# Optimization experiments

Measured on AMD Instinct MI355X. Metric: run time of the kernel, lower is better.

## Reference

```python
import jax, jax.numpy as jnp
import numpy as np

N_NODES = 20000
LN_EPS = 1e-5


def setup_inputs() -> dict:
    key = jax.random.key(0)
    ks = jax.random.split(key, 8)
    N, E, D_IN, D_H = N_NODES, 320000, 128, 256
    x = jax.random.normal(ks[0], (N, D_IN), dtype=jnp.float32)
    edge_index = jax.random.randint(ks[1], (2, E), 0, N, dtype=jnp.int64)
    edge_weight = jax.random.uniform(ks[2], (E,), dtype=jnp.float32)
    # Glorot-ish scaled weights
    W1 = jax.random.normal(ks[3], (D_IN, D_H), dtype=jnp.float32) / np.sqrt(D_IN)
    W2 = jax.random.normal(ks[4], (D_H, D_H), dtype=jnp.float32) / np.sqrt(D_H)
    Wres = jax.random.normal(ks[5], (D_IN, D_H), dtype=jnp.float32) / np.sqrt(D_IN)
    return {
        "x": x, "edge_index": edge_index, "edge_weight": edge_weight,
        "W1": W1, "b1": jnp.zeros((D_H,), jnp.float32),
        "W2": W2, "b2": jnp.zeros((D_H,), jnp.float32),
        "Wres": Wres, "bres": jnp.zeros((D_H,), jnp.float32),
        "gamma1": jnp.ones((D_H,), jnp.float32), "beta1": jnp.zeros((D_H,), jnp.float32),
        "gamma2": jnp.ones((D_H,), jnp.float32), "beta2": jnp.zeros((D_H,), jnp.float32),
    }


def _gcn_conv(x, W, b, src, dst, w, n):
    # PyG GCNConv: linear transform, then sym-normalized scatter-add aggregation
    h = x @ W  # [N, D_H]
    deg = jax.ops.segment_sum(w, dst, num_segments=n)  # in-degree incl. self loops
    dinv = jnp.where(deg > 0, jax.lax.rsqrt(deg), 0.0)
    norm = dinv[src] * w * dinv[dst]  # [E+N]
    out = jax.ops.segment_sum(norm[:, None] * h[src], dst, num_segments=n)
    return out + b


def _layer_norm(x, gamma, beta):
    mu = jnp.mean(x, axis=-1, keepdims=True)
    var = jnp.mean(jnp.square(x - mu), axis=-1, keepdims=True)
    return (x - mu) * jax.lax.rsqrt(var + LN_EPS) * gamma + beta


def reference(x, edge_index, edge_weight, W1, b1, W2, b2, Wres, bres,
              gamma1, beta1, gamma2, beta2):
    n = x.shape[0]
    loop = jnp.arange(n, dtype=edge_index.dtype)
    # add self loops with weight 1 (add_self_loops=True)
    src = jnp.concatenate([edge_index[0], loop])
    dst = jnp.concatenate([edge_index[1], loop])
    w = jnp.concatenate([edge_weight, jnp.ones((n,), edge_weight.dtype)])

    # hop 0: conv -> relu (dropout p=0, eval) -> residual proj -> LayerNorm
    delta = jax.nn.relu(_gcn_conv(x, W1, b1, src, dst, w, n))
    h = _layer_norm(x @ Wres + bres + delta, gamma1, beta1)

    # hop 1 (last): conv -> residual -> LayerNorm (no relu)
    delta = _gcn_conv(h, W2, b2, src, dst, w, n)
    h = _layer_norm(h + delta, gamma2, beta2)
    return h
```

## Files before the change

kernel.cpp:

```cpp
#include <hip/hip_runtime.h>
#include <stdint.h>


constexpr int DIN = 128;
constexpr int DH  = 256;
#define LN_EPS 1e-5f

typedef __attribute__((ext_vector_type(8))) short bf16x8;
typedef __attribute__((ext_vector_type(4))) short bf16x4;
typedef __attribute__((ext_vector_type(4))) float f32x4;

__device__ __forceinline__ short f2bf(float f) {
  union { float f; unsigned u; } v; v.f = f;
  unsigned r = v.u + 0x7fffu + ((v.u >> 16) & 1u);
  return (short)(r >> 16);
}
__device__ __forceinline__ float bf2f(short b) {
  union { unsigned u; float f; } v; v.u = ((unsigned)(unsigned short)b) << 16;
  return v.f;
}

__device__ __forceinline__ int probe_m64(const unsigned* ei, int E) {
  int lane = threadIdx.x & 63;
  long long stride = (E >= 64) ? (E / 64) : 1;
  long long li = (long long)lane * stride;
  if (li >= E) li = 0;
  unsigned v = ei[2 * li + 1];
  return __ballot(v != 0u) == 0ull;
}

__device__ __forceinline__ int eidx(const void* ei, long long e, int m64) {
  return m64 ? (int)((const long long*)ei)[e] : ((const int*)ei)[e];
}


__global__ __launch_bounds__(256) void k_prep(const float* __restrict__ x,
                                              short* __restrict__ xb,
                                              const float* __restrict__ W1,
                                              const float* __restrict__ Wres,
                                              const float* __restrict__ W2,
                                              short* __restrict__ W1t,
                                              short* __restrict__ Wrt,
                                              short* __restrict__ W2t,
                                              const void* ei,
                                              const float* __restrict__ ew,
                                              float* deg, int* cnt,
                                              int N, int E) {
  const int NXV = N * DIN / 8;
  const int NW  = DIN * DH;
  const int NW2 = DH * DH;
  int idx = blockIdx.x * 256 + threadIdx.x;
  if (idx < NXV) {
    f32x4 a = ((const f32x4*)x)[idx * 2];
    f32x4 b = ((const f32x4*)x)[idx * 2 + 1];
    bf16x8 o;
    o[0] = f2bf(a[0]); o[1] = f2bf(a[1]); o[2] = f2bf(a[2]); o[3] = f2bf(a[3]);
    o[4] = f2bf(b[0]); o[5] = f2bf(b[1]); o[6] = f2bf(b[2]); o[7] = f2bf(b[3]);
    ((bf16x8*)xb)[idx] = o;
    return;
  }
  idx -= NXV;
  if (idx < NW) {
    int n = idx / DIN, k = idx % DIN;
    W1t[idx] = f2bf(W1[k * DH + n]);
    return;
  }
  idx -= NW;
  if (idx < NW) {
    int n = idx / DIN, k = idx % DIN;
    Wrt[idx] = f2bf(Wres[k * DH + n]);
    return;
  }
  idx -= NW;
  if (idx < NW2) {
    int n = idx / DH, k = idx % DH;
    W2t[idx] = f2bf(W2[k * DH + n]);
    return;
  }
  idx -= NW2;
  int m64 = probe_m64((const unsigned*)ei, E);
  if (idx < E) {
    int d = eidx(ei, (long long)E + idx, m64);
    atomicAdd(&deg[d], ew[idx]);
    atomicAdd(&cnt[d], 1);
  }
}


__global__ __launch_bounds__(1024) void k_scan(const int* __restrict__ cnt,
                                               float* deg, int* rowptr,
                                               int* cursor, int n) {
  for (int i = threadIdx.x; i < n; i += 1024) deg[i] = rsqrtf(1.0f + deg[i]);

  constexpr int MAXI = 32;
  int items = (n + 1023) / 1024;
  int tid = threadIdx.x, lane = tid & 63, wv = tid >> 6;
  int base = tid * items;
  int v[MAXI];
  int tot = 0;
#pragma unroll 4
  for (int j = 0; j < items; ++j) {
    int i = base + j;
    v[j] = (i < n) ? cnt[i] : 0;
    tot += v[j];
  }
  int sc = tot;
#pragma unroll
  for (int off = 1; off < 64; off <<= 1) {
    int t = __shfl_up(sc, off, 64);
    if (lane >= off) sc += t;
  }
  __shared__ int wsum[16];
  if (lane == 63) wsum[wv] = sc;
  __syncthreads();
  if (wv == 0 && lane < 16) {
    int s = wsum[lane];
#pragma unroll
    for (int off = 1; off < 16; off <<= 1) {
      int t = __shfl_up(s, off, 64);
      if (lane >= off) s += t;
    }
    wsum[lane] = s;
  }
  __syncthreads();
  int prefix = (sc - tot) + ((wv > 0) ? wsum[wv - 1] : 0);
  if (tid == 0) { rowptr[0] = 0; cursor[0] = 0; }
  int run = prefix;
#pragma unroll 4
  for (int j = 0; j < items; ++j) {
    int i = base + j;
    run += v[j];
    if (i < n) { rowptr[i + 1] = run; cursor[i + 1] = run; }
  }
}


__global__ __launch_bounds__(256) void k_gemm_l1_fill(
    const short* __restrict__ A, const short* __restrict__ B1,
    const short* __restrict__ Br, const float* __restrict__ bres,
    short* __restrict__ H1, short* __restrict__ RESb, int M, int MB,
    const void* ei, const float* __restrict__ ew,
    const float* __restrict__ dinv, int* cursor, int* srcs, float* norms,
    int E) {
  constexpr int K = DIN;
  int GB = MB * 4;
  if ((int)blockIdx.x >= GB) {
    int m64 = probe_m64((const unsigned*)ei, E);
    int e = ((int)blockIdx.x - GB) * 256 + threadIdx.x;
    if (e >= E) return;
    int s = eidx(ei, e, m64);
    int d = eidx(ei, (long long)E + e, m64);
    int p = atomicAdd(&cursor[d], 1);
    srcs[p] = s;
    norms[p] = dinv[s] * ew[e] * dinv[d];
    return;
  }
  int mb = (int)blockIdx.x % MB, nbk = (int)blockIdx.x / MB;
  int tid = threadIdx.x;
  int wave = tid >> 6, lane = tid & 63;
  int lr = lane & 15, lg = lane >> 4;
  int bm = mb * 64 + (wave >> 1) * 32;
  int bn = nbk * 64 + (wave & 1) * 32;

  int r0 = min(bm + lr, M - 1);
  int r1 = min(bm + 16 + lr, M - 1);
  const short* a0p = A + (long long)r0 * K + lg * 8;
  const short* a1p = A + (long long)r1 * K + lg * 8;
  const short* b10p = B1 + (long long)(bn + lr) * K + lg * 8;
  const short* b11p = B1 + (long long)(bn + 16 + lr) * K + lg * 8;
  const short* br0p = Br + (long long)(bn + lr) * K + lg * 8;
  const short* br1p = Br + (long long)(bn + 16 + lr) * K + lg * 8;

  f32x4 a1c[2][2] = {}, arc[2][2] = {};
#pragma unroll
  for (int ks = 0; ks < K / 32; ++ks) {
    bf16x8 a0 = *(const bf16x8*)(a0p + ks * 32);
    bf16x8 a1 = *(const bf16x8*)(a1p + ks * 32);
    bf16x8 p0 = *(const bf16x8*)(b10p + ks * 32);
    bf16x8 p1 = *(const bf16x8*)(b11p + ks * 32);
    bf16x8 q0 = *(const bf16x8*)(br0p + ks * 32);
    bf16x8 q1 = *(const bf16x8*)(br1p + ks * 32);
    a1c[0][0] = __builtin_amdgcn_mfma_f32_16x16x32_bf16(a0, p0, a1c[0][0], 0, 0, 0);
    a1c[0][1] = __builtin_amdgcn_mfma_f32_16x16x32_bf16(a0, p1, a1c[0][1], 0, 0, 0);
    a1c[1][0] = __builtin_amdgcn_mfma_f32_16x16x32_bf16(a1, p0, a1c[1][0], 0, 0, 0);
    a1c[1][1] = __builtin_amdgcn_mfma_f32_16x16x32_bf16(a1, p1, a1c[1][1], 0, 0, 0);
    arc[0][0] = __builtin_amdgcn_mfma_f32_16x16x32_bf16(a0, q0, arc[0][0], 0, 0, 0);
    arc[0][1] = __builtin_amdgcn_mfma_f32_16x16x32_bf16(a0, q1, arc[0][1], 0, 0, 0);
    arc[1][0] = __builtin_amdgcn_mfma_f32_16x16x32_bf16(a1, q0, arc[1][0], 0, 0, 0);
    arc[1][1] = __builtin_amdgcn_mfma_f32_16x16x32_bf16(a1, q1, arc[1][1], 0, 0, 0);
  }

#pragma unroll
  for (int mi = 0; mi < 2; ++mi)
#pragma unroll
    for (int ni = 0; ni < 2; ++ni)
#pragma unroll
      for (int j = 0; j < 4; ++j) {
        int row = bm + mi * 16 + lg * 4 + j;
        int col = bn + ni * 16 + lr;
        if (row < M) {
          H1[(long long)row * DH + col] = f2bf(a1c[mi][ni][j]);
          RESb[(long long)row * DH + col] = f2bf(arc[mi][ni][j] + bres[col]);
        }
      }
}


__global__ __launch_bounds__(256) void k_gemm2(const short* __restrict__ A,
                                               const short* __restrict__ Bt,
                                               short* __restrict__ outb, int M) {
  constexpr int K = DH;
  int tid = threadIdx.x;
  int wave = tid >> 6, lane = tid & 63;
  int lr = lane & 15, lg = lane >> 4;
  int bm = blockIdx.x * 64 + (wave >> 1) * 32;
  int bn = blockIdx.y * 64 + (wave & 1) * 32;

  int r0 = min(bm + lr, M - 1);
  int r1 = min(bm + 16 + lr, M - 1);
  const short* a0p = A + (long long)r0 * K + lg * 8;
  const short* a1p = A + (long long)r1 * K + lg * 8;
  const short* b0p = Bt + (long long)(bn + lr) * K + lg * 8;
  const short* b1p = Bt + (long long)(bn + 16 + lr) * K + lg * 8;

  f32x4 acc[2][2] = {};
#pragma unroll
  for (int ks = 0; ks < K / 32; ++ks) {
    bf16x8 a0 = *(const bf16x8*)(a0p + ks * 32);
    bf16x8 a1 = *(const bf16x8*)(a1p + ks * 32);
    bf16x8 b0 = *(const bf16x8*)(b0p + ks * 32);
    bf16x8 b1 = *(const bf16x8*)(b1p + ks * 32);
    acc[0][0] = __builtin_amdgcn_mfma_f32_16x16x32_bf16(a0, b0, acc[0][0], 0, 0, 0);
    acc[0][1] = __builtin_amdgcn_mfma_f32_16x16x32_bf16(a0, b1, acc[0][1], 0, 0, 0);
    acc[1][0] = __builtin_amdgcn_mfma_f32_16x16x32_bf16(a1, b0, acc[1][0], 0, 0, 0);
    acc[1][1] = __builtin_amdgcn_mfma_f32_16x16x32_bf16(a1, b1, acc[1][1], 0, 0, 0);
  }

#pragma unroll
  for (int mi = 0; mi < 2; ++mi)
#pragma unroll
    for (int ni = 0; ni < 2; ++ni)
#pragma unroll
      for (int j = 0; j < 4; ++j) {
        int row = bm + mi * 16 + lg * 4 + j;
        int col = bn + ni * 16 + lr;
        if (row < M) outb[(long long)row * DH + col] = f2bf(acc[mi][ni][j]);
      }
}


template <bool RELU, bool RESBF>
__global__ __launch_bounds__(256) void k_agg_ln(
    const short* __restrict__ H, const void* __restrict__ resid,
    const float* __restrict__ bias, const float* __restrict__ gamma,
    const float* __restrict__ beta, const int* __restrict__ rowptr,
    const int* __restrict__ srcs, const float* __restrict__ norms,
    const float* __restrict__ dinv, float* __restrict__ out_f,
    short* __restrict__ out_bf, int n) {
  int wv = threadIdx.x >> 6, lane = threadIdx.x & 63;
  int i = blockIdx.x * 4 + wv;
  if (i >= n) return;
  int d = lane * 4;

  float di = dinv[i];
  float acc0, acc1, acc2, acc3;
  {
    bf16x4 hv = *(const bf16x4*)(H + (long long)i * DH + d);
    float sw = di * di;
    acc0 = sw * bf2f(hv[0]); acc1 = sw * bf2f(hv[1]);
    acc2 = sw * bf2f(hv[2]); acc3 = sw * bf2f(hv[3]);
  }
  int e = rowptr[i], end = rowptr[i + 1];
  for (; e + 8 <= end; e += 8) {
    int s0 = srcs[e],     s1 = srcs[e + 1], s2 = srcs[e + 2], s3 = srcs[e + 3];
    int s4 = srcs[e + 4], s5 = srcs[e + 5], s6 = srcs[e + 6], s7 = srcs[e + 7];
    bf16x4 v0 = *(const bf16x4*)(H + (long long)s0 * DH + d);
    bf16x4 v1 = *(const bf16x4*)(H + (long long)s1 * DH + d);
    bf16x4 v2 = *(const bf16x4*)(H + (long long)s2 * DH + d);
    bf16x4 v3 = *(const bf16x4*)(H + (long long)s3 * DH + d);
    bf16x4 v4 = *(const bf16x4*)(H + (long long)s4 * DH + d);
    bf16x4 v5 = *(const bf16x4*)(H + (long long)s5 * DH + d);
    bf16x4 v6 = *(const bf16x4*)(H + (long long)s6 * DH + d);
    bf16x4 v7 = *(const bf16x4*)(H + (long long)s7 * DH + d);
    float n0 = norms[e],     n1 = norms[e + 1], n2 = norms[e + 2], n3 = norms[e + 3];
    float n4 = norms[e + 4], n5 = norms[e + 5], n6 = norms[e + 6], n7 = norms[e + 7];
    acc0 += n0 * bf2f(v0[0]); acc1 += n0 * bf2f(v0[1]);
    acc2 += n0 * bf2f(v0[2]); acc3 += n0 * bf2f(v0[3]);
    acc0 += n1 * bf2f(v1[0]); acc1 += n1 * bf2f(v1[1]);
    acc2 += n1 * bf2f(v1[2]); acc3 += n1 * bf2f(v1[3]);
    acc0 += n2 * bf2f(v2[0]); acc1 += n2 * bf2f(v2[1]);
    acc2 += n2 * bf2f(v2[2]); acc3 += n2 * bf2f(v2[3]);
    acc0 += n3 * bf2f(v3[0]); acc1 += n3 * bf2f(v3[1]);
    acc2 += n3 * bf2f(v3[2]); acc3 += n3 * bf2f(v3[3]);
    acc0 += n4 * bf2f(v4[0]); acc1 += n4 * bf2f(v4[1]);
    acc2 += n4 * bf2f(v4[2]); acc3 += n4 * bf2f(v4[3]);
    acc0 += n5 * bf2f(v5[0]); acc1 += n5 * bf2f(v5[1]);
    acc2 += n5 * bf2f(v5[2]); acc3 += n5 * bf2f(v5[3]);
    acc0 += n6 * bf2f(v6[0]); acc1 += n6 * bf2f(v6[1]);
    acc2 += n6 * bf2f(v6[2]); acc3 += n6 * bf2f(v6[3]);
    acc0 += n7 * bf2f(v7[0]); acc1 += n7 * bf2f(v7[1]);
    acc2 += n7 * bf2f(v7[2]); acc3 += n7 * bf2f(v7[3]);
  }
  for (; e < end; ++e) {
    int s = srcs[e];
    float nm = norms[e];
    bf16x4 v = *(const bf16x4*)(H + (long long)s * DH + d);
    acc0 += nm * bf2f(v[0]); acc1 += nm * bf2f(v[1]);
    acc2 += nm * bf2f(v[2]); acc3 += nm * bf2f(v[3]);
  }

  float r0, r1, r2, r3;
  if (RESBF) {
    bf16x4 rv = *(const bf16x4*)((const short*)resid + (long long)i * DH + d);
    r0 = bf2f(rv[0]); r1 = bf2f(rv[1]); r2 = bf2f(rv[2]); r3 = bf2f(rv[3]);
  } else {
    f32x4 rv = *(const f32x4*)((const float*)resid + (long long)i * DH + d);
    r0 = rv[0]; r1 = rv[1]; r2 = rv[2]; r3 = rv[3];
  }
  f32x4 bv = *(const f32x4*)(bias + d);
  float t0 = acc0 + bv[0], t1 = acc1 + bv[1], t2 = acc2 + bv[2], t3 = acc3 + bv[3];
  if (RELU) {
    t0 = fmaxf(t0, 0.f); t1 = fmaxf(t1, 0.f);
    t2 = fmaxf(t2, 0.f); t3 = fmaxf(t3, 0.f);
  }
  t0 += r0; t1 += r1; t2 += r2; t3 += r3;

  float s1 = t0 + t1 + t2 + t3;
  float s2 = t0 * t0 + t1 * t1 + t2 * t2 + t3 * t3;
#pragma unroll
  for (int m = 1; m < 64; m <<= 1) {
    s1 += __shfl_xor(s1, m, 64);
    s2 += __shfl_xor(s2, m, 64);
  }
  float mu = s1 * (1.f / 256.f);
  float var = s2 * (1.f / 256.f) - mu * mu;
  float rs = rsqrtf(var + LN_EPS);

  f32x4 gv = *(const f32x4*)(gamma + d);
  f32x4 be = *(const f32x4*)(beta + d);
  f32x4 y;
  y[0] = (t0 - mu) * rs * gv[0] + be[0];
  y[1] = (t1 - mu) * rs * gv[1] + be[1];
  y[2] = (t2 - mu) * rs * gv[2] + be[2];
  y[3] = (t3 - mu) * rs * gv[3] + be[3];
  if (out_f) *(f32x4*)(out_f + (long long)i * DH + d) = y;
  if (out_bf) {
    bf16x4 ob;
    ob[0] = f2bf(y[0]); ob[1] = f2bf(y[1]);
    ob[2] = f2bf(y[2]); ob[3] = f2bf(y[3]);
    *(bf16x4*)(out_bf + (long long)i * DH + d) = ob;
  }
}


extern "C" void kernel_launch(void* const* d_in, const int* in_sizes, int n_in,
                              void* d_out, int out_size, void* d_ws,
                              size_t ws_size, hipStream_t stream) {
  const float* x    = (const float*)d_in[0];
  const void*  ei   = d_in[1];
  const float* ew   = (const float*)d_in[2];
  const float* W1   = (const float*)d_in[3];
  const float* b1   = (const float*)d_in[4];
  const float* W2   = (const float*)d_in[5];
  const float* b2   = (const float*)d_in[6];
  const float* Wres = (const float*)d_in[7];
  const float* bres = (const float*)d_in[8];
  const float* g1   = (const float*)d_in[9];
  const float* be1  = (const float*)d_in[10];
  const float* g2   = (const float*)d_in[11];
  const float* be2  = (const float*)d_in[12];

  const int N = in_sizes[0] / DIN;
  const int E = in_sizes[2];

  char* ws = (char*)d_ws;
  auto alloc = [&](size_t bytes) -> char* {
    char* p = ws;
    ws += (bytes + 255) & ~(size_t)255;
    return p;
  };
  short* xb     = (short*)alloc((size_t)N * DIN * 2);
  short* W1t    = (short*)alloc((size_t)DIN * DH * 2);
  short* Wrt    = (short*)alloc((size_t)DIN * DH * 2);
  short* W2t    = (short*)alloc((size_t)DH * DH * 2);
  short* Hb     = (short*)alloc((size_t)N * DH * 2);
  short* RESb   = (short*)alloc((size_t)N * DH * 2);
  short* h1b    = (short*)alloc((size_t)N * DH * 2);
  int*   cnt    = (int*)alloc((size_t)N * 8);
  float* deg    = (float*)(cnt + N);
  int*   rowptr = (int*)alloc((size_t)(N + 1) * 4);
  int*   cursor = (int*)alloc((size_t)(N + 1) * 4);
  int*   srcs   = (int*)alloc((size_t)E * 4);
  float* norms  = (float*)alloc((size_t)E * 4);

  hipMemsetAsync(cnt, 0, (size_t)N * 8, stream);

  int prep_items = N * DIN / 8 + 2 * DIN * DH + DH * DH + E;
  k_prep<<<(prep_items + 255) / 256, 256, 0, stream>>>(
      x, xb, W1, Wres, W2, W1t, Wrt, W2t, ei, ew, deg, cnt, N, E);
  k_scan<<<1, 1024, 0, stream>>>(cnt, deg, rowptr, cursor, N);

  const int MB = (N + 63) / 64;
  const int FB = (E + 255) / 256;
  k_gemm_l1_fill<<<MB * 4 + FB, 256, 0, stream>>>(
      xb, W1t, Wrt, bres, Hb, RESb, N, MB, ei, ew, deg, cursor, srcs, norms, E);
  k_agg_ln<true, true><<<(N + 3) / 4, 256, 0, stream>>>(
      Hb, RESb, b1, g1, be1, rowptr, srcs, norms, deg, nullptr, h1b, N);

  dim3 gg(MB, DH / 64);
  k_gemm2<<<gg, 256, 0, stream>>>(h1b, W2t, Hb, N);
  k_agg_ln<false, true><<<(N + 3) / 4, 256, 0, stream>>>(
      Hb, h1b, b2, g2, be2, rowptr, srcs, norms, deg, (float*)d_out, nullptr, N);
}
```

Before: 265.1 us.

## Aggregate before transform and fuse GEMM with bias, residual and LayerNorm

Reorders each GCN layer so aggregation runs first, using linearity (A·X·W = (A·X)·W). For layer 1 this gathers the 128-wide input instead of the 256-wide hidden, halving gather traffic. The dense GEMMs now use one wave per 16 rows covering all 256 columns, so bias, ReLU, the residual projection and LayerNorm all finish in registers, with no HBM round-trip for intermediates or separate aggregation+LN kernels. The CSR fill moves to its own kernel, and the aggregation kernels split each row's edges across two half-waves. The trade-offs are low-occupancy 64-thread GEMM blocks that reload weights from global memory per block, and bf16 rounding of the aggregated features.

```diff
diff --git a/kernel.cpp b/kernel.cpp
--- a/kernel.cpp
+++ b/kernel.cpp
@@ -135,220 +135,233 @@
 }
 
 
-__global__ __launch_bounds__(256) void k_gemm_l1_fill(
-    const short* __restrict__ A, const short* __restrict__ B1,
-    const short* __restrict__ Br, const float* __restrict__ bres,
-    short* __restrict__ H1, short* __restrict__ RESb, int M, int MB,
-    const void* ei, const float* __restrict__ ew,
-    const float* __restrict__ dinv, int* cursor, int* srcs, float* norms,
-    int E) {
-  constexpr int K = DIN;
-  int GB = MB * 4;
-  if ((int)blockIdx.x >= GB) {
-    int m64 = probe_m64((const unsigned*)ei, E);
-    int e = ((int)blockIdx.x - GB) * 256 + threadIdx.x;
-    if (e >= E) return;
-    int s = eidx(ei, e, m64);
-    int d = eidx(ei, (long long)E + e, m64);
-    int p = atomicAdd(&cursor[d], 1);
-    srcs[p] = s;
-    norms[p] = dinv[s] * ew[e] * dinv[d];
-    return;
-  }
-  int mb = (int)blockIdx.x % MB, nbk = (int)blockIdx.x / MB;
-  int tid = threadIdx.x;
-  int wave = tid >> 6, lane = tid & 63;
-  int lr = lane & 15, lg = lane >> 4;
-  int bm = mb * 64 + (wave >> 1) * 32;
-  int bn = nbk * 64 + (wave & 1) * 32;
-
-  int r0 = min(bm + lr, M - 1);
-  int r1 = min(bm + 16 + lr, M - 1);
-  const short* a0p = A + (long long)r0 * K + lg * 8;
-  const short* a1p = A + (long long)r1 * K + lg * 8;
-  const short* b10p = B1 + (long long)(bn + lr) * K + lg * 8;
-  const short* b11p = B1 + (long long)(bn + 16 + lr) * K + lg * 8;
-  const short* br0p = Br + (long long)(bn + lr) * K + lg * 8;
-  const short* br1p = Br + (long long)(bn + 16 + lr) * K + lg * 8;
-
-  f32x4 a1c[2][2] = {}, arc[2][2] = {};
-#pragma unroll
-  for (int ks = 0; ks < K / 32; ++ks) {
-    bf16x8 a0 = *(const bf16x8*)(a0p + ks * 32);
-    bf16x8 a1 = *(const bf16x8*)(a1p + ks * 32);
-    bf16x8 p0 = *(const bf16x8*)(b10p + ks * 32);
-    bf16x8 p1 = *(const bf16x8*)(b11p + ks * 32);
-    bf16x8 q0 = *(const bf16x8*)(br0p + ks * 32);
-    bf16x8 q1 = *(const bf16x8*)(br1p + ks * 32);
-    a1c[0][0] = __builtin_amdgcn_mfma_f32_16x16x32_bf16(a0, p0, a1c[0][0], 0, 0, 0);
-    a1c[0][1] = __builtin_amdgcn_mfma_f32_16x16x32_bf16(a0, p1, a1c[0][1], 0, 0, 0);
-    a1c[1][0] = __builtin_amdgcn_mfma_f32_16x16x32_bf16(a1, p0, a1c[1][0], 0, 0, 0);
-    a1c[1][1] = __builtin_amdgcn_mfma_f32_16x16x32_bf16(a1, p1, a1c[1][1], 0, 0, 0);
-    arc[0][0] = __builtin_amdgcn_mfma_f32_16x16x32_bf16(a0, q0, arc[0][0], 0, 0, 0);
-    arc[0][1] = __builtin_amdgcn_mfma_f32_16x16x32_bf16(a0, q1, arc[0][1], 0, 0, 0);
-    arc[1][0] = __builtin_amdgcn_mfma_f32_16x16x32_bf16(a1, q0, arc[1][0], 0, 0, 0);
-    arc[1][1] = __builtin_amdgcn_mfma_f32_16x16x32_bf16(a1, q1, arc[1][1], 0, 0, 0);
-  }
-
-#pragma unroll
-  for (int mi = 0; mi < 2; ++mi)
-#pragma unroll
-    for (int ni = 0; ni < 2; ++ni)
-#pragma unroll
-      for (int j = 0; j < 4; ++j) {
-        int row = bm + mi * 16 + lg * 4 + j;
-        int col = bn + ni * 16 + lr;
-        if (row < M) {
-          H1[(long long)row * DH + col] = f2bf(a1c[mi][ni][j]);
-          RESb[(long long)row * DH + col] = f2bf(arc[mi][ni][j] + bres[col]);
-        }
-      }
-}
-
-
-__global__ __launch_bounds__(256) void k_gemm2(const short* __restrict__ A,
-                                               const short* __restrict__ Bt,
-                                               short* __restrict__ outb, int M) {
-  constexpr int K = DH;
-  int tid = threadIdx.x;
-  int wave = tid >> 6, lane = tid & 63;
-  int lr = lane & 15, lg = lane >> 4;
-  int bm = blockIdx.x * 64 + (wave >> 1) * 32;
-  int bn = blockIdx.y * 64 + (wave & 1) * 32;
-
-  int r0 = min(bm + lr, M - 1);
-  int r1 = min(bm + 16 + lr, M - 1);
-  const short* a0p = A + (long long)r0 * K + lg * 8;
-  const short* a1p = A + (long long)r1 * K + lg * 8;
-  const short* b0p = Bt + (long long)(bn + lr) * K + lg * 8;
-  const short* b1p = Bt + (long long)(bn + 16 + lr) * K + lg * 8;
-
-  f32x4 acc[2][2] = {};
-#pragma unroll
-  for (int ks = 0; ks < K / 32; ++ks) {
-    bf16x8 a0 = *(const bf16x8*)(a0p + ks * 32);
-    bf16x8 a1 = *(const bf16x8*)(a1p + ks * 32);
-    bf16x8 b0 = *(const bf16x8*)(b0p + ks * 32);
-    bf16x8 b1 = *(const bf16x8*)(b1p + ks * 32);
-    acc[0][0] = __builtin_amdgcn_mfma_f32_16x16x32_bf16(a0, b0, acc[0][0], 0, 0, 0);
-    acc[0][1] = __builtin_amdgcn_mfma_f32_16x16x32_bf16(a0, b1, acc[0][1], 0, 0, 0);
-    acc[1][0] = __builtin_amdgcn_mfma_f32_16x16x32_bf16(a1, b0, acc[1][0], 0, 0, 0);
-    acc[1][1] = __builtin_amdgcn_mfma_f32_16x16x32_bf16(a1, b1, acc[1][1], 0, 0, 0);
-  }
-
-#pragma unroll
-  for (int mi = 0; mi < 2; ++mi)
-#pragma unroll
-    for (int ni = 0; ni < 2; ++ni)
-#pragma unroll
-      for (int j = 0; j < 4; ++j) {
-        int row = bm + mi * 16 + lg * 4 + j;
-        int col = bn + ni * 16 + lr;
-        if (row < M) outb[(long long)row * DH + col] = f2bf(acc[mi][ni][j]);
-      }
-}
-
-
-template <bool RELU, bool RESBF>
-__global__ __launch_bounds__(256) void k_agg_ln(
-    const short* __restrict__ H, const void* __restrict__ resid,
-    const float* __restrict__ bias, const float* __restrict__ gamma,
-    const float* __restrict__ beta, const int* __restrict__ rowptr,
-    const int* __restrict__ srcs, const float* __restrict__ norms,
-    const float* __restrict__ dinv, float* __restrict__ out_f,
-    short* __restrict__ out_bf, int n) {
+__global__ __launch_bounds__(256) void k_fill(const void* ei,
+                                              const float* __restrict__ w,
+                                              const float* __restrict__ dinv,
+                                              int* cursor, int* srcs,
+                                              float* norms, int E) {
+  int m64 = probe_m64((const unsigned*)ei, E);
+  int e = blockIdx.x * 256 + threadIdx.x;
+  if (e >= E) return;
+  int s = eidx(ei, e, m64);
+  int d = eidx(ei, (long long)E + e, m64);
+  int p = atomicAdd(&cursor[d], 1);
+  srcs[p] = s;
+  norms[p] = dinv[s] * w[e] * dinv[d];
+}
+
+
+__global__ __launch_bounds__(256) void k_agg128(const short* __restrict__ T,
+                                                const int* __restrict__ rowptr,
+                                                const int* __restrict__ srcs,
+                                                const float* __restrict__ norms,
+                                                const float* __restrict__ dinv,
+                                                short* __restrict__ out, int n) {
   int wv = threadIdx.x >> 6, lane = threadIdx.x & 63;
   int i = blockIdx.x * 4 + wv;
   if (i >= n) return;
-  int d = lane * 4;
-
-  float di = dinv[i];
-  float acc0, acc1, acc2, acc3;
-  {
-    bf16x4 hv = *(const bf16x4*)(H + (long long)i * DH + d);
-    float sw = di * di;
-    acc0 = sw * bf2f(hv[0]); acc1 = sw * bf2f(hv[1]);
-    acc2 = sw * bf2f(hv[2]); acc3 = sw * bf2f(hv[3]);
-  }
-  int e = rowptr[i], end = rowptr[i + 1];
-  for (; e + 8 <= end; e += 8) {
-    int s0 = srcs[e],     s1 = srcs[e + 1], s2 = srcs[e + 2], s3 = srcs[e + 3];
-    int s4 = srcs[e + 4], s5 = srcs[e + 5], s6 = srcs[e + 6], s7 = srcs[e + 7];
-    bf16x4 v0 = *(const bf16x4*)(H + (long long)s0 * DH + d);
-    bf16x4 v1 = *(const bf16x4*)(H + (long long)s1 * DH + d);
-    bf16x4 v2 = *(const bf16x4*)(H + (long long)s2 * DH + d);
-    bf16x4 v3 = *(const bf16x4*)(H + (long long)s3 * DH + d);
-    bf16x4 v4 = *(const bf16x4*)(H + (long long)s4 * DH + d);
-    bf16x4 v5 = *(const bf16x4*)(H + (long long)s5 * DH + d);
-    bf16x4 v6 = *(const bf16x4*)(H + (long long)s6 * DH + d);
-    bf16x4 v7 = *(const bf16x4*)(H + (long long)s7 * DH + d);
-    float n0 = norms[e],     n1 = norms[e + 1], n2 = norms[e + 2], n3 = norms[e + 3];
-    float n4 = norms[e + 4], n5 = norms[e + 5], n6 = norms[e + 6], n7 = norms[e + 7];
-    acc0 += n0 * bf2f(v0[0]); acc1 += n0 * bf2f(v0[1]);
-    acc2 += n0 * bf2f(v0[2]); acc3 += n0 * bf2f(v0[3]);
-    acc0 += n1 * bf2f(v1[0]); acc1 += n1 * bf2f(v1[1]);
-    acc2 += n1 * bf2f(v1[2]); acc3 += n1 * bf2f(v1[3]);
-    acc0 += n2 * bf2f(v2[0]); acc1 += n2 * bf2f(v2[1]);
-    acc2 += n2 * bf2f(v2[2]); acc3 += n2 * bf2f(v2[3]);
-    acc0 += n3 * bf2f(v3[0]); acc1 += n3 * bf2f(v3[1]);
-    acc2 += n3 * bf2f(v3[2]); acc3 += n3 * bf2f(v3[3]);
-    acc0 += n4 * bf2f(v4[0]); acc1 += n4 * bf2f(v4[1]);
-    acc2 += n4 * bf2f(v4[2]); acc3 += n4 * bf2f(v4[3]);
-    acc0 += n5 * bf2f(v5[0]); acc1 += n5 * bf2f(v5[1]);
-    acc2 += n5 * bf2f(v5[2]); acc3 += n5 * bf2f(v5[3]);
-    acc0 += n6 * bf2f(v6[0]); acc1 += n6 * bf2f(v6[1]);
-    acc2 += n6 * bf2f(v6[2]); acc3 += n6 * bf2f(v6[3]);
-    acc0 += n7 * bf2f(v7[0]); acc1 += n7 * bf2f(v7[1]);
-    acc2 += n7 * bf2f(v7[2]); acc3 += n7 * bf2f(v7[3]);
-  }
-  for (; e < end; ++e) {
+  int h = lane >> 5;
+  int c = (lane & 31) * 4;
+  float a0 = 0.f, a1 = 0.f, a2 = 0.f, a3 = 0.f;
+  int e = rowptr[i] + h, end = rowptr[i + 1];
+  for (; e + 6 < end; e += 8) {
+    int s0 = srcs[e], s1 = srcs[e + 2], s2 = srcs[e + 4], s3 = srcs[e + 6];
+    float w0 = norms[e], w1 = norms[e + 2], w2 = norms[e + 4], w3 = norms[e + 6];
+    bf16x4 v0 = *(const bf16x4*)(T + (long long)s0 * DIN + c);
+    bf16x4 v1 = *(const bf16x4*)(T + (long long)s1 * DIN + c);
+    bf16x4 v2 = *(const bf16x4*)(T + (long long)s2 * DIN + c);
+    bf16x4 v3 = *(const bf16x4*)(T + (long long)s3 * DIN + c);
+    a0 += w0 * bf2f(v0[0]) + w1 * bf2f(v1[0]) + w2 * bf2f(v2[0]) + w3 * bf2f(v3[0]);
+    a1 += w0 * bf2f(v0[1]) + w1 * bf2f(v1[1]) + w2 * bf2f(v2[1]) + w3 * bf2f(v3[1]);
+    a2 += w0 * bf2f(v0[2]) + w1 * bf2f(v1[2]) + w2 * bf2f(v2[2]) + w3 * bf2f(v3[2]);
+    a3 += w0 * bf2f(v0[3]) + w1 * bf2f(v1[3]) + w2 * bf2f(v2[3]) + w3 * bf2f(v3[3]);
+  }
+  for (; e < end; e += 2) {
     int s = srcs[e];
-    float nm = norms[e];
-    bf16x4 v = *(const bf16x4*)(H + (long long)s * DH + d);
-    acc0 += nm * bf2f(v[0]); acc1 += nm * bf2f(v[1]);
-    acc2 += nm * bf2f(v[2]); acc3 += nm * bf2f(v[3]);
-  }
-
-  float r0, r1, r2, r3;
-  if (RESBF) {
-    bf16x4 rv = *(const bf16x4*)((const short*)resid + (long long)i * DH + d);
-    r0 = bf2f(rv[0]); r1 = bf2f(rv[1]); r2 = bf2f(rv[2]); r3 = bf2f(rv[3]);
-  } else {
-    f32x4 rv = *(const f32x4*)((const float*)resid + (long long)i * DH + d);
-    r0 = rv[0]; r1 = rv[1]; r2 = rv[2]; r3 = rv[3];
-  }
-  f32x4 bv = *(const f32x4*)(bias + d);
-  float t0 = acc0 + bv[0], t1 = acc1 + bv[1], t2 = acc2 + bv[2], t3 = acc3 + bv[3];
-  if (RELU) {
-    t0 = fmaxf(t0, 0.f); t1 = fmaxf(t1, 0.f);
-    t2 = fmaxf(t2, 0.f); t3 = fmaxf(t3, 0.f);
-  }
-  t0 += r0; t1 += r1; t2 += r2; t3 += r3;
-
-  float s1 = t0 + t1 + t2 + t3;
-  float s2 = t0 * t0 + t1 * t1 + t2 * t2 + t3 * t3;
-#pragma unroll
-  for (int m = 1; m < 64; m <<= 1) {
-    s1 += __shfl_xor(s1, m, 64);
-    s2 += __shfl_xor(s2, m, 64);
-  }
-  float mu = s1 * (1.f / 256.f);
-  float var = s2 * (1.f / 256.f) - mu * mu;
-  float rs = rsqrtf(var + LN_EPS);
-
-  f32x4 gv = *(const f32x4*)(gamma + d);
-  f32x4 be = *(const f32x4*)(beta + d);
-  f32x4 y;
-  y[0] = (t0 - mu) * rs * gv[0] + be[0];
-  y[1] = (t1 - mu) * rs * gv[1] + be[1];
-  y[2] = (t2 - mu) * rs * gv[2] + be[2];
-  y[3] = (t3 - mu) * rs * gv[3] + be[3];
-  if (out_f) *(f32x4*)(out_f + (long long)i * DH + d) = y;
-  if (out_bf) {
-    bf16x4 ob;
-    ob[0] = f2bf(y[0]); ob[1] = f2bf(y[1]);
-    ob[2] = f2bf(y[2]); ob[3] = f2bf(y[3]);
-    *(bf16x4*)(out_bf + (long long)i * DH + d) = ob;
+    float w = norms[e];
+    bf16x4 v = *(const bf16x4*)(T + (long long)s * DIN + c);
+    a0 += w * bf2f(v[0]); a1 += w * bf2f(v[1]);
+    a2 += w * bf2f(v[2]); a3 += w * bf2f(v[3]);
+  }
+  a0 += __shfl_xor(a0, 32, 64); a1 += __shfl_xor(a1, 32, 64);
+  a2 += __shfl_xor(a2, 32, 64); a3 += __shfl_xor(a3, 32, 64);
+  if (h == 0) {
+    float sw = dinv[i] * dinv[i];
+    bf16x4 sv = *(const bf16x4*)(T + (long long)i * DIN + c);
+    bf16x4 o;
+    o[0] = f2bf(a0 + sw * bf2f(sv[0]));
+    o[1] = f2bf(a1 + sw * bf2f(sv[1]));
+    o[2] = f2bf(a2 + sw * bf2f(sv[2]));
+    o[3] = f2bf(a3 + sw * bf2f(sv[3]));
+    *(bf16x4*)(out + (long long)i * DIN + c) = o;
+  }
+}
+
+__global__ __launch_bounds__(256) void k_agg256(const short* __restrict__ T,
+                                                const int* __restrict__ rowptr,
+                                                const int* __restrict__ srcs,
+                                                const float* __restrict__ norms,
+                                                const float* __restrict__ dinv,
+                                                short* __restrict__ out, int n) {
+  int wv = threadIdx.x >> 6, lane = threadIdx.x & 63;
+  int i = blockIdx.x * 4 + wv;
+  if (i >= n) return;
+  int h = lane >> 5;
+  int c = (lane & 31) * 8;
+  float acc[8];
+#pragma unroll
+  for (int k = 0; k < 8; ++k) acc[k] = 0.f;
+  int e = rowptr[i] + h, end = rowptr[i + 1];
+  for (; e + 6 < end; e += 8) {
+    int s0 = srcs[e], s1 = srcs[e + 2], s2 = srcs[e + 4], s3 = srcs[e + 6];
+    float w0 = norms[e], w1 = norms[e + 2], w2 = norms[e + 4], w3 = norms[e + 6];
+    bf16x8 v0 = *(const bf16x8*)(T + (long long)s0 * DH + c);
+    bf16x8 v1 = *(const bf16x8*)(T + (long long)s1 * DH + c);
+    bf16x8 v2 = *(const bf16x8*)(T + (long long)s2 * DH + c);
+    bf16x8 v3 = *(const bf16x8*)(T + (long long)s3 * DH + c);
+#pragma unroll
+    for (int k = 0; k < 8; ++k)
+      acc[k] += w0 * bf2f(v0[k]) + w1 * bf2f(v1[k]) +
+                w2 * bf2f(v2[k]) + w3 * bf2f(v3[k]);
+  }
+  for (; e < end; e += 2) {
+    int s = srcs[e];
+    float w = norms[e];
+    bf16x8 v = *(const bf16x8*)(T + (long long)s * DH + c);
+#pragma unroll
+    for (int k = 0; k < 8; ++k) acc[k] += w * bf2f(v[k]);
+  }
+#pragma unroll
+  for (int k = 0; k < 8; ++k) acc[k] += __shfl_xor(acc[k], 32, 64);
+  if (h == 0) {
+    float sw = dinv[i] * dinv[i];
+    bf16x8 sv = *(const bf16x8*)(T + (long long)i * DH + c);
+    bf16x8 o;
+#pragma unroll
+    for (int k = 0; k < 8; ++k) o[k] = f2bf(acc[k] + sw * bf2f(sv[k]));
+    *(bf16x8*)(out + (long long)i * DH + c) = o;
+  }
+}
+
+
+__global__ __launch_bounds__(64) void k_gemm_ln1(
+    const short* __restrict__ Sx, const short* __restrict__ xb,
+    const short* __restrict__ W1t, const short* __restrict__ Wrt,
+    const float* __restrict__ b1, const float* __restrict__ bres,
+    const float* __restrict__ g1, const float* __restrict__ be1,
+    short* __restrict__ h1b, int M) {
+  int lane = threadIdx.x & 63;
+  int lr = lane & 15, lg = lane >> 4;
+  int bm = blockIdx.x * 16;
+  int ar = min(bm + lr, M - 1);
+
+  f32x4 acc[16] = {};
+#pragma unroll
+  for (int ks = 0; ks < 4; ++ks) {
+    bf16x8 a = *(const bf16x8*)(Sx + (long long)ar * DIN + ks * 32 + lg * 8);
+#pragma unroll
+    for (int ni = 0; ni < 16; ++ni) {
+      bf16x8 b = *(const bf16x8*)(W1t + (ni * 16 + lr) * DIN + ks * 32 + lg * 8);
+      acc[ni] = __builtin_amdgcn_mfma_f32_16x16x32_bf16(a, b, acc[ni], 0, 0, 0);
+    }
+  }
+#pragma unroll
+  for (int ni = 0; ni < 16; ++ni) {
+    int col = ni * 16 + lr;
+    float bb = b1[col], br = bres[col];
+#pragma unroll
+    for (int j = 0; j < 4; ++j)
+      acc[ni][j] = fmaxf(acc[ni][j] + bb, 0.f) + br;
+  }
+#pragma unroll
+  for (int ks = 0; ks < 4; ++ks) {
+    bf16x8 a = *(const bf16x8*)(xb + (long long)ar * DIN + ks * 32 + lg * 8);
+#pragma unroll
+    for (int ni = 0; ni < 16; ++ni) {
+      bf16x8 b = *(const bf16x8*)(Wrt + (ni * 16 + lr) * DIN + ks * 32 + lg * 8);
+      acc[ni] = __builtin_amdgcn_mfma_f32_16x16x32_bf16(a, b, acc[ni], 0, 0, 0);
+    }
+  }
+#pragma unroll
+  for (int j = 0; j < 4; ++j) {
+    int r = bm + lg * 4 + j;
+    float s1 = 0.f, s2 = 0.f;
+#pragma unroll
+    for (int ni = 0; ni < 16; ++ni) {
+      float v = acc[ni][j];
+      s1 += v; s2 += v * v;
+    }
+#pragma unroll
+    for (int m = 1; m < 16; m <<= 1) {
+      s1 += __shfl_xor(s1, m, 64);
+      s2 += __shfl_xor(s2, m, 64);
+    }
+    float mu = s1 * (1.f / 256.f);
+    float rs = rsqrtf(s2 * (1.f / 256.f) - mu * mu + LN_EPS);
+    if (r < M) {
+#pragma unroll
+      for (int ni = 0; ni < 16; ++ni) {
+        int col = ni * 16 + lr;
+        float y = (acc[ni][j] - mu) * rs * g1[col] + be1[col];
+        h1b[(long long)r * DH + col] = f2bf(y);
+      }
+    }
+  }
+}
+
+
+__global__ __launch_bounds__(64) void k_gemm_ln2(
+    const short* __restrict__ Sh1, const short* __restrict__ h1b,
+    const short* __restrict__ W2t, const float* __restrict__ b2,
+    const float* __restrict__ g2, const float* __restrict__ be2,
+    float* __restrict__ out, int M) {
+  int lane = threadIdx.x & 63;
+  int lr = lane & 15, lg = lane >> 4;
+  int bm = blockIdx.x * 16;
+  int ar = min(bm + lr, M - 1);
+
+  f32x4 acc[16] = {};
+#pragma unroll
+  for (int ks = 0; ks < 8; ++ks) {
+    bf16x8 a = *(const bf16x8*)(Sh1 + (long long)ar * DH + ks * 32 + lg * 8);
+#pragma unroll
+    for (int ni = 0; ni < 16; ++ni) {
+      bf16x8 b = *(const bf16x8*)(W2t + (ni * 16 + lr) * DH + ks * 32 + lg * 8);
+      acc[ni] = __builtin_amdgcn_mfma_f32_16x16x32_bf16(a, b, acc[ni], 0, 0, 0);
+    }
+  }
+#pragma unroll
+  for (int j = 0; j < 4; ++j) {
+    int rr = min(bm + lg * 4 + j, M - 1);
+#pragma unroll
+    for (int ni = 0; ni < 16; ++ni) {
+      int col = ni * 16 + lr;
+      acc[ni][j] += b2[col] + bf2f(h1b[(long long)rr * DH + col]);
+    }
+  }
+#pragma unroll
+  for (int j = 0; j < 4; ++j) {
+    int r = bm + lg * 4 + j;
+    float s1 = 0.f, s2 = 0.f;
+#pragma unroll
+    for (int ni = 0; ni < 16; ++ni) {
+      float v = acc[ni][j];
+      s1 += v; s2 += v * v;
+    }
+#pragma unroll
+    for (int m = 1; m < 16; m <<= 1) {
+      s1 += __shfl_xor(s1, m, 64);
+      s2 += __shfl_xor(s2, m, 64);
+    }
+    float mu = s1 * (1.f / 256.f);
+    float rs = rsqrtf(s2 * (1.f / 256.f) - mu * mu + LN_EPS);
+    if (r < M) {
+#pragma unroll
+      for (int ni = 0; ni < 16; ++ni) {
+        int col = ni * 16 + lr;
+        out[(long long)r * DH + col] = (acc[ni][j] - mu) * rs * g2[col] + be2[col];
+      }
+    }
   }
 }
 
@@ -383,9 +396,9 @@
   short* W1t    = (short*)alloc((size_t)DIN * DH * 2);
   short* Wrt    = (short*)alloc((size_t)DIN * DH * 2);
   short* W2t    = (short*)alloc((size_t)DH * DH * 2);
-  short* Hb     = (short*)alloc((size_t)N * DH * 2);
-  short* RESb   = (short*)alloc((size_t)N * DH * 2);
+  short* Sx     = (short*)alloc((size_t)N * DIN * 2);
   short* h1b    = (short*)alloc((size_t)N * DH * 2);
+  short* Sh1    = (short*)alloc((size_t)N * DH * 2);
   int*   cnt    = (int*)alloc((size_t)N * 8);
   float* deg    = (float*)(cnt + N);
   int*   rowptr = (int*)alloc((size_t)(N + 1) * 4);
@@ -399,16 +412,12 @@
   k_prep<<<(prep_items + 255) / 256, 256, 0, stream>>>(
       x, xb, W1, Wres, W2, W1t, Wrt, W2t, ei, ew, deg, cnt, N, E);
   k_scan<<<1, 1024, 0, stream>>>(cnt, deg, rowptr, cursor, N);
-
-  const int MB = (N + 63) / 64;
-  const int FB = (E + 255) / 256;
-  k_gemm_l1_fill<<<MB * 4 + FB, 256, 0, stream>>>(
-      xb, W1t, Wrt, bres, Hb, RESb, N, MB, ei, ew, deg, cursor, srcs, norms, E);
-  k_agg_ln<true, true><<<(N + 3) / 4, 256, 0, stream>>>(
-      Hb, RESb, b1, g1, be1, rowptr, srcs, norms, deg, nullptr, h1b, N);
-
-  dim3 gg(MB, DH / 64);
-  k_gemm2<<<gg, 256, 0, stream>>>(h1b, W2t, Hb, N);
-  k_agg_ln<false, true><<<(N + 3) / 4, 256, 0, stream>>>(
-      Hb, h1b, b2, g2, be2, rowptr, srcs, norms, deg, (float*)d_out, nullptr, N);
-}
+  k_fill<<<(E + 255) / 256, 256, 0, stream>>>(ei, ew, deg, cursor, srcs, norms, E);
+
+  k_agg128<<<(N + 3) / 4, 256, 0, stream>>>(xb, rowptr, srcs, norms, deg, Sx, N);
+  k_gemm_ln1<<<(N + 15) / 16, 64, 0, stream>>>(Sx, xb, W1t, Wrt, b1, bres, g1,
+                                               be1, h1b, N);
+  k_agg256<<<(N + 3) / 4, 256, 0, stream>>>(h1b, rowptr, srcs, norms, deg, Sh1, N);
+  k_gemm_ln2<<<(N + 15) / 16, 64, 0, stream>>>(Sh1, h1b, W2t, b2, g2, be2,
+                                               (float*)d_out, N);
+}
```

Result: no change. 262.5 us (-1.0%).
